# Kernel optimization log

Measured on AMD Instinct MI355X. Metric: run time of the kernel, lower is better.

## Reference

```python
import jax, jax.numpy as jnp
import numpy as np

B, N, A = 32, 1024, 256          # batch, n_entities, n_agents
D_IN, D_H, H = 256, 256, 8       # input_dim, hidden_dim, n_heads
SCALE = 1.0 / np.sqrt(D_H)
EPS = 1e-12


def setup_inputs() -> dict:
    key = jax.random.key(0)
    ks = jax.random.split(key, 7)
    x = jax.random.normal(ks[0], (B, N, D_IN), dtype=jnp.float32)
    # binary visibility mask [batch, n_agents, n_entities]
    m = (jax.random.uniform(ks[1], (B, A, N)) > 0.5).astype(jnp.float32)
    # encoder Linear(input_dim, hidden_dim): weight [out,in], bias [out]
    W_enc = jax.random.normal(ks[2], (D_H, D_IN), dtype=jnp.float32) / np.sqrt(D_IN)
    b_enc = jnp.zeros((D_H,), dtype=jnp.float32)
    # per-head projection matrices stacked [H, D_H, D_H] (torch.randn init)
    WQ = jax.random.normal(ks[3], (H, D_H, D_H), dtype=jnp.float32)
    WK = jax.random.normal(ks[4], (H, D_H, D_H), dtype=jnp.float32)
    WV = jax.random.normal(ks[5], (H, D_H, D_H), dtype=jnp.float32)
    return {"x": x, "m": m, "W_enc": W_enc, "b_enc": b_enc, "WQ": WQ, "WK": WK, "WV": WV}


def reference(x, m, W_enc, b_enc, WQ, WK, WV):
    # encode: LeakyReLU then Linear
    h = jnp.einsum('bni,oi->bno', jax.nn.leaky_relu(x), W_enc) + b_enc  # [B,N,D_H]
    n_agents = m.shape[1]
    ha = h[:, :n_agents]                                   # [B,A,D_H]
    # per-head projections, heads vectorized
    Q = jnp.einsum('bad,hde->bhae', ha, WQ)                # [B,H,A,D_H]
    K = jnp.einsum('bnd,hde->bhne', h, WK)                 # [B,H,N,D_H]
    V = jnp.einsum('bnd,hde->bhne', h, WV)                 # [B,H,N,D_H]
    S = jnp.einsum('bhae,bhne->bhan', Q, K) * SCALE        # [B,H,A,N]
    P = jax.nn.softmax(S, axis=-1)
    P = P * m[:, None]                                     # post-softmax mask
    prob = P / (jnp.sum(P, axis=-1, keepdims=True) + EPS)  # renormalize
    z = jnp.einsum('bhan,bhne->bhae', prob, V)             # [B,H,A,D_H]
    return jnp.mean(z, axis=1)                             # [B,A,D_H]
```

## Files before the change

### kernel.cpp

```cpp
#include <hip/hip_runtime.h>
#include <math.h>

namespace {
constexpr int B_N  = 32;
constexpr int SEQ  = 1024;
constexpr int AG   = 256;
constexpr int D    = 256;
constexpr int NH   = 8;
constexpr float SCALE = 0.0625f;
constexpr float EPS   = 1e-12f;

constexpr size_t HHI_OFF  = 0;
constexpr size_t HLO_OFF  = 16777216;
constexpr size_t HT_OFF   = 33554432;
constexpr size_t MTHI_OFF = 50331648;
constexpr size_t MTLO_OFF = 51380224;
constexpr size_t MB_OFF   = 52428800;
constexpr size_t WVT_OFF  = 53477376;
constexpr size_t Z16_OFF  = 54525952;
}

typedef __attribute__((ext_vector_type(8))) short short8;
typedef __attribute__((ext_vector_type(4))) float floatx4;
#define MFMA_BF(A,B,C) __builtin_amdgcn_mfma_f32_16x16x32_bf16(A,B,C,0,0,0)

__device__ __forceinline__ unsigned short bf16_rtne(float f) {
    unsigned u = __float_as_uint(f);
    u += 0x7fffu + ((u >> 16) & 1u);
    return (unsigned short)(u >> 16);
}
__device__ __forceinline__ float bf16_tof(unsigned short h) {
    return __uint_as_float(((unsigned)h) << 16);
}
__device__ __forceinline__ void async16(void* lds, const void* g) {
    __builtin_amdgcn_global_load_lds(
        (const __attribute__((address_space(1))) unsigned int*)g,
        (__attribute__((address_space(3))) unsigned int*)lds,
        16, 0, 0);
}

__global__ __launch_bounds__(256) void enc_mfma(
    const float* __restrict__ x, const float* __restrict__ W_enc,
    const float* __restrict__ b_enc,
    ushort* __restrict__ h_hi, ushort* __restrict__ h_lo,
    ushort* __restrict__ hT)
{
    __shared__ ushort Ah[64][40], Al[64][40];
    __shared__ ushort Bh[64][40], Bl[64][40];
    __shared__ ushort Th[64][72], Tl[64][72];

    const int t    = threadIdx.x;
    const int wv   = t >> 6;
    const int lane = t & 63;
    const int l15  = lane & 15;
    const int quad = lane >> 4;
    const int col0 = blockIdx.x * 64;
    const int row0 = blockIdx.y * 64;

    floatx4 acc[4];
#pragma unroll
    for (int i = 0; i < 4; ++i) acc[i] = (floatx4){0.f, 0.f, 0.f, 0.f};

    for (int k0 = 0; k0 < 256; k0 += 32) {
        __syncthreads();
        {
            const int r = t >> 2, s = (t & 3) * 8;
            float f[8];
            *(float4*)&f[0] = *(const float4*)(x + (size_t)(row0 + r) * 256 + k0 + s);
            *(float4*)&f[4] = *(const float4*)(x + (size_t)(row0 + r) * 256 + k0 + s + 4);
            short8 hi8, lo8;
#pragma unroll
            for (int e = 0; e < 8; ++e) {
                float v = f[e] > 0.f ? f[e] : 0.01f * f[e];
                unsigned short hb = bf16_rtne(v);
                hi8[e] = (short)hb;
                lo8[e] = (short)bf16_rtne(v - bf16_tof(hb));
            }
            *(short8*)&Ah[r][s] = hi8;
            *(short8*)&Al[r][s] = lo8;
            *(float4*)&f[0] = *(const float4*)(W_enc + (size_t)(col0 + r) * 256 + k0 + s);
            *(float4*)&f[4] = *(const float4*)(W_enc + (size_t)(col0 + r) * 256 + k0 + s + 4);
#pragma unroll
            for (int e = 0; e < 8; ++e) {
                unsigned short hb = bf16_rtne(f[e]);
                hi8[e] = (short)hb;
                lo8[e] = (short)bf16_rtne(f[e] - bf16_tof(hb));
            }
            *(short8*)&Bh[r][s] = hi8;
            *(short8*)&Bl[r][s] = lo8;
        }
        __syncthreads();

        short8 Af  = *(const short8*)&Ah[wv * 16 + l15][quad * 8];
        short8 Afl = *(const short8*)&Al[wv * 16 + l15][quad * 8];
#pragma unroll
        for (int et = 0; et < 4; ++et) {
            short8 Bf  = *(const short8*)&Bh[et * 16 + l15][quad * 8];
            short8 Bfl = *(const short8*)&Bl[et * 16 + l15][quad * 8];
            acc[et] = MFMA_BF(Af,  Bf,  acc[et]);
            acc[et] = MFMA_BF(Afl, Bf,  acc[et]);
            acc[et] = MFMA_BF(Af,  Bfl, acc[et]);
        }
    }

    __syncthreads();
#pragma unroll
    for (int et = 0; et < 4; ++et) {
        const int col = et * 16 + l15;
        const float bb = b_enc[col0 + col];
#pragma unroll
        for (int r = 0; r < 4; ++r) {
            const int row = wv * 16 + quad * 4 + r;
            const float v = acc[et][r] + bb;
            const unsigned short hb = bf16_rtne(v);
            Th[row][col] = hb;
            Tl[row][col] = bf16_rtne(v - bf16_tof(hb));
        }
    }
    __syncthreads();
    {
        const int r = t >> 2, c0 = (t & 3) * 16;
        ushort* dh = h_hi + (size_t)(row0 + r) * 256 + col0 + c0;
        ushort* dl = h_lo + (size_t)(row0 + r) * 256 + col0 + c0;
        *(short8*)dh       = *(const short8*)&Th[r][c0];
        *(short8*)(dh + 8) = *(const short8*)&Th[r][c0 + 8];
        *(short8*)dl       = *(const short8*)&Tl[r][c0];
        *(short8*)(dl + 8) = *(const short8*)&Tl[r][c0 + 8];
    }
    {
        const int bq = (int)blockIdx.y >> 4;
        const int n0 = ((int)blockIdx.y & 15) * 64;
        const int dd = t >> 2, seg = (t & 3) * 16;
        ushort tmp[16];
#pragma unroll
        for (int j = 0; j < 16; ++j) tmp[j] = Th[seg + j][dd];
        ushort* dst = hT + ((size_t)(bq * 256 + col0 + dd)) * 1024 + n0 + seg;
        *(short8*)dst       = *(short8*)&tmp[0];
        *(short8*)(dst + 8) = *(short8*)&tmp[8];
    }
}

__global__ __launch_bounds__(256) void prep_fused(
    const float* __restrict__ m, unsigned* __restrict__ mb,
    const float* __restrict__ WV, ushort* __restrict__ WVt,
    const float* __restrict__ WQ, const float* __restrict__ WK,
    ushort* __restrict__ Mt_hi, ushort* __restrict__ Mt_lo)
{
    __shared__ __align__(16) char plds[17408];
    const int t = threadIdx.x;
    const int v = blockIdx.x;

    if (v < 1024) {
        const int idx = v * 256 + t;
        const float4* src = (const float4*)(m + (size_t)idx * 32);
        unsigned wbits = 0;
#pragma unroll
        for (int i = 0; i < 8; ++i) {
            float4 vv = src[i];
            wbits |= (vv.x > 0.5f ? 1u : 0u) << (i * 4 + 0);
            wbits |= (vv.y > 0.5f ? 1u : 0u) << (i * 4 + 1);
            wbits |= (vv.z > 0.5f ? 1u : 0u) << (i * 4 + 2);
            wbits |= (vv.w > 0.5f ? 1u : 0u) << (i * 4 + 3);
        }
        mb[idx] = wbits;
    } else if (v < 1152) {
        float (*T)[68] = (float(*)[68])plds;
        const int v2 = v - 1024;
        const int d0 = (v2 & 3) * 64, e0 = ((v2 >> 2) & 3) * 64, h = v2 >> 4;
        {
            const int r = t >> 2, c = (t & 3) * 16;
            const float* src = WV + ((size_t)(h * 256 + d0 + r)) * 256 + e0 + c;
#pragma unroll
            for (int j = 0; j < 4; ++j)
                *(float4*)&T[r][c + j * 4] = *(const float4*)(src + j * 4);
        }
        __syncthreads();
        {
            const int ee = t >> 2, seg = (t & 3) * 16;
            ushort tmp[16];
#pragma unroll
            for (int j = 0; j < 16; ++j) tmp[j] = bf16_rtne(T[seg + j][ee]);
            ushort* dst = WVt + ((size_t)(h * 256 + e0 + ee)) * 256 + d0 + seg;
            *(short8*)dst       = *(short8*)&tmp[0];
            *(short8*)(dst + 8) = *(short8*)&tmp[8];
        }
    } else {
        float (*AsT)[68] = (float(*)[68])plds;
        float (*BsT)[68] = (float(*)[68])(plds + 8704);
        const int v3 = v - 1152;
        const int tx = t & 15, ty = t >> 4;
        const int col0 = (v3 & 3) * 64;
        const int row0 = ((v3 >> 2) & 3) * 64;
        const int hz   = v3 >> 4;
        const float* A  = WK + (size_t)hz * 256 * 256;
        const float* Bm = WQ + (size_t)hz * 256 * 256;
        ushort* Chi = Mt_hi + (size_t)hz * 256 * 256;
        ushort* Clo = Mt_lo + (size_t)hz * 256 * 256;

        float acc[4][4];
#pragma unroll
        for (int r = 0; r < 4; ++r)
#pragma unroll
            for (int c = 0; c < 4; ++c) acc[r][c] = 0.f;

        for (int k0 = 0; k0 < 256; k0 += 32) {
            __syncthreads();
#pragma unroll
            for (int ss = 0; ss < 2; ++ss) {
                int flat = t + 256 * ss;
                int rr = flat >> 3, k4 = flat & 7;
                float4 vv = *(const float4*)(A + (size_t)(row0 + rr) * 256 + k0 + k4 * 4);
                AsT[k4*4+0][rr] = vv.x; AsT[k4*4+1][rr] = vv.y;
                AsT[k4*4+2][rr] = vv.z; AsT[k4*4+3][rr] = vv.w;
                float4 wv = *(const float4*)(Bm + (size_t)(col0 + rr) * 256 + k0 + k4 * 4);
                BsT[k4*4+0][rr] = wv.x; BsT[k4*4+1][rr] = wv.y;
                BsT[k4*4+2][rr] = wv.z; BsT[k4*4+3][rr] = wv.w;
            }
            __syncthreads();
#pragma unroll 8
            for (int kk = 0; kk < 32; ++kk) {
                float4 a4 = *(const float4*)&AsT[kk][ty * 4];
                float4 b4 = *(const float4*)&BsT[kk][tx * 4];
                const float ar[4] = {a4.x, a4.y, a4.z, a4.w};
                const float bc[4] = {b4.x, b4.y, b4.z, b4.w};
#pragma unroll
                for (int r = 0; r < 4; ++r)
#pragma unroll
                    for (int c = 0; c < 4; ++c)
                        acc[r][c] = fmaf(ar[r], bc[c], acc[r][c]);
            }
        }
#pragma unroll
        for (int r = 0; r < 4; ++r) {
            const int row = row0 + ty * 4 + r;
            ushort hi4[4], lo4[4];
#pragma unroll
            for (int c = 0; c < 4; ++c) {
                float vv = acc[r][c];
                hi4[c] = bf16_rtne(vv);
                lo4[c] = bf16_rtne(vv - bf16_tof(hi4[c]));
            }
            *(ushort4*)(Chi + (size_t)row * 256 + col0 + tx * 4) =
                make_ushort4(hi4[0], hi4[1], hi4[2], hi4[3]);
            *(ushort4*)(Clo + (size_t)row * 256 + col0 + tx * 4) =
                make_ushort4(lo4[0], lo4[1], lo4[2], lo4[3]);
        }
    }
}

__global__ __launch_bounds__(512, 2) void attn_mfma(
    const ushort* __restrict__ h_hi, const ushort* __restrict__ h_lo,
    const ushort* __restrict__ hT,   const ushort* __restrict__ Mt_hi,
    const ushort* __restrict__ Mt_lo, const unsigned* __restrict__ mbits,
    ushort* __restrict__ zout)
{
    __shared__ __align__(16) char lds[118784];
    ushort* pP = (ushort*)(lds + 98304);
    ushort* pE = (ushort*)(lds + 108544);

    const int t    = threadIdx.x;
    const int wv   = t >> 6;
    const int lane = t & 63;
    const int l15  = lane & 15;
    const int quad = lane >> 4;
    const int f    = blockIdx.x;
    const int b    = (f & 7) + 8 * (f >> 7);
    const int mid  = (f >> 3) & 15;
    const int hh   = (mid >> 2) * 2 + (wv >> 2);
    const int a0   = (mid & 3) * 64;
    const int aw   = a0 + (wv & 3) * 16;

    const ushort* hbh = h_hi + (size_t)b * SEQ * D;
    const ushort* hbl = h_lo + (size_t)b * SEQ * D;
    const ushort* hTb = hT   + (size_t)b * D * SEQ;

    floatx4 qac[16];
#pragma unroll
    for (int i = 0; i < 16; ++i) qac[i] = (floatx4){0.f, 0.f, 0.f, 0.f};

    for (int kc = 0; kc < 4; ++kc) {
        short8 Ah[2], Al[2];
#pragma unroll
        for (int kt = 0; kt < 2; ++kt) {
            const size_t ao = ((size_t)b * SEQ + aw + l15) * D +
                              kc * 64 + kt * 32 + quad * 8;
            Ah[kt] = *(const short8*)(h_hi + ao);
            Al[kt] = *(const short8*)(h_lo + ao);
        }
#pragma unroll
        for (int nt2 = 0; nt2 < 16; ++nt2) {
#pragma unroll
            for (int kt = 0; kt < 2; ++kt) {
                const size_t mo = ((size_t)hh * D + nt2 * 16 + l15) * D +
                                  kc * 64 + kt * 32 + quad * 8;
                short8 Bh = *(const short8*)(Mt_hi + mo);
                short8 Bl = *(const short8*)(Mt_lo + mo);
                qac[nt2] = MFMA_BF(Ah[kt], Bh, qac[nt2]);
                qac[nt2] = MFMA_BF(Al[kt], Bh, qac[nt2]);
                qac[nt2] = MFMA_BF(Ah[kt], Bl, qac[nt2]);
            }
        }
    }

    short8 Qhi[8], Qlo[8];
    {
        float* qscr = (float*)lds;
        for (int c = 0; c < 4; ++c) {
#pragma unroll
            for (int j = 0; j < 4; ++j)
#pragma unroll
                for (int r = 0; r < 4; ++r)
                    qscr[(wv * 16 + quad * 4 + r) * 68 + j * 16 + l15] = qac[c * 4 + j][r];
#pragma unroll
            for (int kt = 0; kt < 2; ++kt) {
                const float* pr = &qscr[(wv * 16 + l15) * 68 + kt * 32 + quad * 8];
                float ftmp[8];
                *(float4*)&ftmp[0] = *(const float4*)pr;
                *(float4*)&ftmp[4] = *(const float4*)(pr + 4);
                short8 hi, lo;
#pragma unroll
                for (int e = 0; e < 8; ++e) {
                    unsigned short hb = bf16_rtne(ftmp[e]);
                    hi[e] = (short)hb;
                    lo[e] = (short)bf16_rtne(ftmp[e] - bf16_tof(hb));
                }
                Qhi[c * 2 + kt] = hi;
                Qlo[c * 2 + kt] = lo;
            }
        }
    }
    __syncthreads();

    auto issue_tile = [&](char* buf, int n0) {
        ushort* dh = (ushort*)buf;
        ushort* dl = (ushort*)(buf + 16384);
        ushort* dT = (ushort*)(buf + 32768);
#pragma unroll
        for (int i = 0; i < 2; ++i) {
            const int slot = wv * 128 + i * 64 + lane;
            const int row  = slot >> 5;
            const int p    = slot & 31;
            const int c    = p ^ (row & 7);
            const size_t go = (size_t)(n0 + row) * 256 + c * 8;
            const size_t lo_ = (size_t)(wv * 128 + i * 64) * 8;
            async16(dh + lo_, hbh + go);
            async16(dl + lo_, hbl + go);
        }
#pragma unroll
        for (int i = 0; i < 2; ++i) {
            const int slot = wv * 128 + i * 64 + lane;
            const int row  = slot >> 2;
            const int p    = slot & 3;
            const int c    = p ^ ((row >> 2) & 3);
            async16(dT + (size_t)(wv * 128 + i * 64) * 8,
                    hTb + (size_t)row * 1024 + n0 + c * 8);
        }
    };

    issue_tile(lds,         0);
    issue_tile(lds + 49152, 32);
    __syncthreads();

    floatx4 zac[16];
#pragma unroll
    for (int i = 0; i < 16; ++i) zac[i] = (floatx4){0.f, 0.f, 0.f, 0.f};
    floatx4 zacZ = (floatx4){0.f, 0.f, 0.f, 0.f};
    floatx4 zacE = (floatx4){0.f, 0.f, 0.f, 0.f};
    float mx[4] = {-INFINITY, -INFINITY, -INFINITY, -INFINITY};

    short8 onesf;
#pragma unroll
    for (int e = 0; e < 8; ++e) onesf[e] = (short)0x3F80;

    const unsigned* mbr = mbits + ((size_t)b * AG + aw + quad * 4) * (SEQ / 32);

    for (int nt = 0; nt < 32; ++nt) {
        char* cur = lds + (size_t)(nt & 1) * 49152;
        ushort* hS_hi = (ushort*)cur;
        ushort* hS_lo = (ushort*)(cur + 16384);
        ushort* hTS   = (ushort*)(cur + 32768);

        floatx4 sacH[2], sacL[2];
        sacH[0] = (floatx4){0.f, 0.f, 0.f, 0.f};
        sacH[1] = (floatx4){0.f, 0.f, 0.f, 0.f};
        sacL[0] = (floatx4){0.f, 0.f, 0.f, 0.f};
        sacL[1] = (floatx4){0.f, 0.f, 0.f, 0.f};
#pragma unroll
        for (int ks = 0; ks < 8; ++ks) {
            const int cg = ks * 4 + quad;
#pragma unroll
            for (int ntile = 0; ntile < 2; ++ntile) {
                const int row = ntile * 16 + l15;
                const int off = row * 256 + (cg ^ (row & 7)) * 8;
                short8 Bh = *(const short8*)&hS_hi[off];
                short8 Bl = *(const short8*)&hS_lo[off];
                sacH[ntile] = MFMA_BF(Qhi[ks], Bh, sacH[ntile]);
                sacL[ntile] = MFMA_BF(Qlo[ks], Bh, sacL[ntile]);
                sacL[ntile] = MFMA_BF(Qhi[ks], Bl, sacL[ntile]);
            }
        }

        float l0[4], l1[4];
#pragma unroll
        for (int r = 0; r < 4; ++r) {
            l0[r] = (sacH[0][r] + sacL[0][r]) * SCALE;
            l1[r] = (sacH[1][r] + sacL[1][r]) * SCALE;
        }

        float mt[4];
#pragma unroll
        for (int r = 0; r < 4; ++r) mt[r] = fmaxf(l0[r], l1[r]);
#pragma unroll
        for (int off = 1; off < 16; off <<= 1) {
#pragma unroll
            for (int r = 0; r < 4; ++r)
                mt[r] = fmaxf(mt[r], __shfl_xor(mt[r], off));
        }

        const bool need = (mt[0] > mx[0] + 8.0f) || (mt[1] > mx[1] + 8.0f) ||
                          (mt[2] > mx[2] + 8.0f) || (mt[3] > mx[3] + 8.0f);
        if (__any(need)) {
            float alr[4];
#pragma unroll
            for (int r = 0; r < 4; ++r) {
                const float mxn = fmaxf(mx[r], mt[r]);
                alr[r] = __expf(mx[r] - mxn);
                mx[r] = mxn;
            }
#pragma unroll
            for (int dt = 0; dt < 16; ++dt) {
                zac[dt][0] *= alr[0]; zac[dt][1] *= alr[1];
                zac[dt][2] *= alr[2]; zac[dt][3] *= alr[3];
            }
            zacZ[0] *= alr[0]; zacZ[1] *= alr[1];
            zacZ[2] *= alr[2]; zacZ[3] *= alr[3];
            zacE[0] *= alr[0]; zacE[1] *= alr[1];
            zacE[2] *= alr[2]; zacE[3] *= alr[3];
        }

#pragma unroll
        for (int r = 0; r < 4; ++r) {
            const unsigned w0 = mbr[r * (SEQ / 32) + nt];
            const float e0 = __expf(l0[r] - mx[r]);
            const float e1 = __expf(l1[r] - mx[r]);
            const float p0 = ((w0 >> l15) & 1u)        ? e0 : 0.f;
            const float p1 = ((w0 >> (16 + l15)) & 1u) ? e1 : 0.f;
            const int row = wv * 16 + quad * 4 + r;
            pP[row * 40 + l15]      = bf16_rtne(p0);
            pP[row * 40 + 16 + l15] = bf16_rtne(p1);
            pE[row * 40 + l15]      = bf16_rtne(e0);
            pE[row * 40 + 16 + l15] = bf16_rtne(e1);
        }

        short8 Pf = *(const short8*)&pP[(wv * 16 + l15) * 40 + quad * 8];
        short8 Ef = *(const short8*)&pE[(wv * 16 + l15) * 40 + quad * 8];
        zacZ = MFMA_BF(Pf, onesf, zacZ);
        zacE = MFMA_BF(Ef, onesf, zacE);

#pragma unroll
        for (int dt = 0; dt < 16; ++dt) {
            const int row = dt * 16 + l15;
            const int p   = quad ^ ((row >> 2) & 3);
            short8 Bf = *(const short8*)&hTS[row * 32 + p * 8];
            zac[dt] = MFMA_BF(Pf, Bf, zac[dt]);
        }

        __syncthreads();
        if (nt + 2 < 32) issue_tile(cur, (nt + 2) * 32);
    }

#pragma unroll
    for (int r = 0; r < 4; ++r) {
        const int a = aw + quad * 4 + r;
        const float inv = 1.0f / (zacZ[r] + EPS * zacE[r]);
        ushort* zr = zout + (((size_t)b * NH + hh) * AG + a) * D;
#pragma unroll
        for (int dt = 0; dt < 16; ++dt)
            zr[dt * 16 + l15] = bf16_rtne(zac[dt][r] * inv);
    }
}

__global__ __launch_bounds__(256) void out_mfma(
    const ushort* __restrict__ z16, const ushort* __restrict__ WVt,
    float* __restrict__ out)
{
    const int t    = threadIdx.x;
    const int wv   = t >> 6;
    const int lane = t & 63;
    const int l15  = lane & 15;
    const int quad = lane >> 4;
    const int e0 = blockIdx.x * 64;
    const int a0 = blockIdx.y * 64;
    const int b  = blockIdx.z;
    const int aw = a0 + wv * 16;

    floatx4 acc[4];
#pragma unroll
    for (int i = 0; i < 4; ++i) acc[i] = (floatx4){0.f, 0.f, 0.f, 0.f};

#pragma unroll 4
    for (int c = 0; c < 64; ++c) {
        const int hh = c >> 3, d0 = (c & 7) * 32;
        short8 Af = *(const short8*)(z16 +
            (((size_t)b * NH + hh) * AG + aw + l15) * D + d0 + quad * 8);
#pragma unroll
        for (int et = 0; et < 4; ++et) {
            short8 Bf = *(const short8*)(WVt +
                ((size_t)hh * D + e0 + et * 16 + l15) * D + d0 + quad * 8);
            acc[et] = MFMA_BF(Af, Bf, acc[et]);
        }
    }
#pragma unroll
    for (int et = 0; et < 4; ++et)
#pragma unroll
        for (int r = 0; r < 4; ++r)
            out[((size_t)b * AG + aw + quad * 4 + r) * D + e0 + et * 16 + l15] =
                acc[et][r] * 0.125f;
}

extern "C" void kernel_launch(void* const* d_in, const int* in_sizes, int n_in,
                              void* d_out, int out_size, void* d_ws, size_t ws_size,
                              hipStream_t stream)
{
    (void)in_sizes; (void)n_in; (void)out_size; (void)ws_size;
    const float* x     = (const float*)d_in[0];
    const float* m     = (const float*)d_in[1];
    const float* W_enc = (const float*)d_in[2];
    const float* b_enc = (const float*)d_in[3];
    const float* WQ    = (const float*)d_in[4];
    const float* WK    = (const float*)d_in[5];
    const float* WV    = (const float*)d_in[6];
    float* out = (float*)d_out;
    char* ws = (char*)d_ws;

    ushort*   h_hi  = (ushort*)(ws + HHI_OFF);
    ushort*   h_lo  = (ushort*)(ws + HLO_OFF);
    ushort*   hT    = (ushort*)(ws + HT_OFF);
    ushort*   Mt_hi = (ushort*)(ws + MTHI_OFF);
    ushort*   Mt_lo = (ushort*)(ws + MTLO_OFF);
    unsigned* mbits = (unsigned*)(ws + MB_OFF);
    ushort*   WVt   = (ushort*)(ws + WVT_OFF);
    ushort*   z16   = (ushort*)(ws + Z16_OFF);

    enc_mfma<<<dim3(4, 512, 1), dim3(256), 0, stream>>>(
        x, W_enc, b_enc, h_hi, h_lo, hT);
    prep_fused<<<dim3(1280, 1, 1), dim3(256), 0, stream>>>(
        m, mbits, WV, WVt, WQ, WK, Mt_hi, Mt_lo);
    attn_mfma<<<dim3(512, 1, 1), dim3(512), 0, stream>>>(
        h_hi, h_lo, hT, Mt_hi, Mt_lo, mbits, z16);
    out_mfma<<<dim3(4, 4, B_N), dim3(256), 0, stream>>>(z16, WVt, out);
}
```

Baseline: 528.8 us.

## Double entity tile to 64 and read V-transpose fragments directly from global

The attention loop now handles 64 entities per step instead of 32, which halves the number of iterations and block-wide barriers. It computes four score tiles and issues two P·V MFMAs per output tile. The transposed-h tile is no longer staged in LDS; its B fragments are loaded straight from global memory inside the MFMA loop. The P and E staging buffers now share one LDS region. This cuts LDS traffic and barriers, but exposes global-load latency in the inner loop and needs a larger LDS allocation.

```diff
diff --git a/kernel.cpp b/kernel.cpp
--- a/kernel.cpp
+++ b/kernel.cpp
@@ -254,9 +254,8 @@
     const ushort* __restrict__ Mt_lo, const unsigned* __restrict__ mbits,
     ushort* __restrict__ zout)
 {
-    __shared__ __align__(16) char lds[118784];
-    ushort* pP = (ushort*)(lds + 98304);
-    ushort* pE = (ushort*)(lds + 108544);
+    __shared__ __align__(16) char lds[149504];
+    ushort* pP = (ushort*)(lds + 131072);
 
     const int t    = threadIdx.x;
     const int wv   = t >> 6;
@@ -333,32 +332,22 @@
 
     auto issue_tile = [&](char* buf, int n0) {
         ushort* dh = (ushort*)buf;
-        ushort* dl = (ushort*)(buf + 16384);
-        ushort* dT = (ushort*)(buf + 32768);
-#pragma unroll
-        for (int i = 0; i < 2; ++i) {
-            const int slot = wv * 128 + i * 64 + lane;
+        ushort* dl = (ushort*)(buf + 32768);
+#pragma unroll
+        for (int i = 0; i < 4; ++i) {
+            const int slot = wv * 256 + i * 64 + lane;
             const int row  = slot >> 5;
             const int p    = slot & 31;
             const int c    = p ^ (row & 7);
-            const size_t go = (size_t)(n0 + row) * 256 + c * 8;
-            const size_t lo_ = (size_t)(wv * 128 + i * 64) * 8;
+            const size_t go  = (size_t)(n0 + row) * 256 + c * 8;
+            const size_t lo_ = (size_t)(wv * 256 + i * 64) * 8;
             async16(dh + lo_, hbh + go);
             async16(dl + lo_, hbl + go);
         }
-#pragma unroll
-        for (int i = 0; i < 2; ++i) {
-            const int slot = wv * 128 + i * 64 + lane;
-            const int row  = slot >> 2;
-            const int p    = slot & 3;
-            const int c    = p ^ ((row >> 2) & 3);
-            async16(dT + (size_t)(wv * 128 + i * 64) * 8,
-                    hTb + (size_t)row * 1024 + n0 + c * 8);
-        }
     };
 
     issue_tile(lds,         0);
-    issue_tile(lds + 49152, 32);
+    issue_tile(lds + 65536, 64);
     __syncthreads();
 
     floatx4 zac[16];
@@ -373,23 +362,25 @@
     for (int e = 0; e < 8; ++e) onesf[e] = (short)0x3F80;
 
     const unsigned* mbr = mbits + ((size_t)b * AG + aw + quad * 4) * (SEQ / 32);
-
-    for (int nt = 0; nt < 32; ++nt) {
-        char* cur = lds + (size_t)(nt & 1) * 49152;
+    const ushort*   hTl = hTb + (size_t)l15 * 1024 + quad * 8;
+
+    for (int nt = 0; nt < 16; ++nt) {
+        const int n0 = nt * 64;
+        char* cur = lds + (size_t)(nt & 1) * 65536;
         ushort* hS_hi = (ushort*)cur;
-        ushort* hS_lo = (ushort*)(cur + 16384);
-        ushort* hTS   = (ushort*)(cur + 32768);
-
-        floatx4 sacH[2], sacL[2];
-        sacH[0] = (floatx4){0.f, 0.f, 0.f, 0.f};
-        sacH[1] = (floatx4){0.f, 0.f, 0.f, 0.f};
-        sacL[0] = (floatx4){0.f, 0.f, 0.f, 0.f};
-        sacL[1] = (floatx4){0.f, 0.f, 0.f, 0.f};
+        ushort* hS_lo = (ushort*)(cur + 32768);
+
+        floatx4 sacH[4], sacL[4];
+#pragma unroll
+        for (int i = 0; i < 4; ++i) {
+            sacH[i] = (floatx4){0.f, 0.f, 0.f, 0.f};
+            sacL[i] = (floatx4){0.f, 0.f, 0.f, 0.f};
+        }
 #pragma unroll
         for (int ks = 0; ks < 8; ++ks) {
             const int cg = ks * 4 + quad;
 #pragma unroll
-            for (int ntile = 0; ntile < 2; ++ntile) {
+            for (int ntile = 0; ntile < 4; ++ntile) {
                 const int row = ntile * 16 + l15;
                 const int off = row * 256 + (cg ^ (row & 7)) * 8;
                 short8 Bh = *(const short8*)&hS_hi[off];
@@ -400,16 +391,17 @@
             }
         }
 
-        float l0[4], l1[4];
-#pragma unroll
-        for (int r = 0; r < 4; ++r) {
-            l0[r] = (sacH[0][r] + sacL[0][r]) * SCALE;
-            l1[r] = (sacH[1][r] + sacL[1][r]) * SCALE;
-        }
+        float ln[4][4];
+#pragma unroll
+        for (int ntile = 0; ntile < 4; ++ntile)
+#pragma unroll
+            for (int r = 0; r < 4; ++r)
+                ln[ntile][r] = (sacH[ntile][r] + sacL[ntile][r]) * SCALE;
 
         float mt[4];
 #pragma unroll
-        for (int r = 0; r < 4; ++r) mt[r] = fmaxf(l0[r], l1[r]);
+        for (int r = 0; r < 4; ++r)
+            mt[r] = fmaxf(fmaxf(ln[0][r], ln[1][r]), fmaxf(ln[2][r], ln[3][r]));
 #pragma unroll
         for (int off = 1; off < 16; off <<= 1) {
 #pragma unroll
@@ -440,33 +432,48 @@
 
 #pragma unroll
         for (int r = 0; r < 4; ++r) {
-            const unsigned w0 = mbr[r * (SEQ / 32) + nt];
-            const float e0 = __expf(l0[r] - mx[r]);
-            const float e1 = __expf(l1[r] - mx[r]);
-            const float p0 = ((w0 >> l15) & 1u)        ? e0 : 0.f;
-            const float p1 = ((w0 >> (16 + l15)) & 1u) ? e1 : 0.f;
-            const int row = wv * 16 + quad * 4 + r;
-            pP[row * 40 + l15]      = bf16_rtne(p0);
-            pP[row * 40 + 16 + l15] = bf16_rtne(p1);
-            pE[row * 40 + l15]      = bf16_rtne(e0);
-            pE[row * 40 + 16 + l15] = bf16_rtne(e1);
-        }
-
-        short8 Pf = *(const short8*)&pP[(wv * 16 + l15) * 40 + quad * 8];
-        short8 Ef = *(const short8*)&pE[(wv * 16 + l15) * 40 + quad * 8];
-        zacZ = MFMA_BF(Pf, onesf, zacZ);
-        zacE = MFMA_BF(Ef, onesf, zacE);
+            const unsigned w0 = mbr[r * 32 + nt * 2];
+            const unsigned w1 = mbr[r * 32 + nt * 2 + 1];
+            const int rowp = (wv * 16 + quad * 4 + r) * 72;
+            const float e0 = __expf(ln[0][r] - mx[r]);
+            const float e1 = __expf(ln[1][r] - mx[r]);
+            const float e2 = __expf(ln[2][r] - mx[r]);
+            const float e3 = __expf(ln[3][r] - mx[r]);
+            pP[rowp      + l15] = bf16_rtne(((w0 >> l15) & 1u)        ? e0 : 0.f);
+            pP[rowp + 16 + l15] = bf16_rtne(((w0 >> (16 + l15)) & 1u) ? e1 : 0.f);
+            pP[rowp + 32 + l15] = bf16_rtne(((w1 >> l15) & 1u)        ? e2 : 0.f);
+            pP[rowp + 48 + l15] = bf16_rtne(((w1 >> (16 + l15)) & 1u) ? e3 : 0.f);
+        }
+
+        short8 Pf0 = *(const short8*)&pP[(wv * 16 + l15) * 72 + quad * 8];
+        short8 Pf1 = *(const short8*)&pP[(wv * 16 + l15) * 72 + 32 + quad * 8];
+
+#pragma unroll
+        for (int r = 0; r < 4; ++r) {
+            const int rowp = (wv * 16 + quad * 4 + r) * 72;
+            pP[rowp      + l15] = bf16_rtne(__expf(ln[0][r] - mx[r]));
+            pP[rowp + 16 + l15] = bf16_rtne(__expf(ln[1][r] - mx[r]));
+            pP[rowp + 32 + l15] = bf16_rtne(__expf(ln[2][r] - mx[r]));
+            pP[rowp + 48 + l15] = bf16_rtne(__expf(ln[3][r] - mx[r]));
+        }
+        short8 Ef0 = *(const short8*)&pP[(wv * 16 + l15) * 72 + quad * 8];
+        short8 Ef1 = *(const short8*)&pP[(wv * 16 + l15) * 72 + 32 + quad * 8];
+
+        zacZ = MFMA_BF(Pf0, onesf, zacZ);
+        zacZ = MFMA_BF(Pf1, onesf, zacZ);
+        zacE = MFMA_BF(Ef0, onesf, zacE);
+        zacE = MFMA_BF(Ef1, onesf, zacE);
 
 #pragma unroll
         for (int dt = 0; dt < 16; ++dt) {
-            const int row = dt * 16 + l15;
-            const int p   = quad ^ ((row >> 2) & 3);
-            short8 Bf = *(const short8*)&hTS[row * 32 + p * 8];
-            zac[dt] = MFMA_BF(Pf, Bf, zac[dt]);
+            short8 Bf0 = *(const short8*)(hTl + (size_t)dt * 16384 + n0);
+            short8 Bf1 = *(const short8*)(hTl + (size_t)dt * 16384 + n0 + 32);
+            zac[dt] = MFMA_BF(Pf0, Bf0, zac[dt]);
+            zac[dt] = MFMA_BF(Pf1, Bf1, zac[dt]);
         }
 
         __syncthreads();
-        if (nt + 2 < 32) issue_tile(cur, (nt + 2) * 32);
+        if (nt + 2 < 16) issue_tile(cur, (nt + 2) * 64);
     }
 
 #pragma unroll
```

Result: slower. 678.2 us (+28.2%).
